# Optimization experiments

Hardware: AMD Instinct MI355X
Metric: run time of the kernel (lower is better)

Reference implementation:

```python
import jax, jax.numpy as jnp
import numpy as np

N_NODES = 50000
X_DIM = 64
EMBED_DIM = 320  # x_dim + hidden*num_hops = 64 + 128*2
N_EDGES = 400000
HIDDEN_MLP = 64
SAMPLE_BIAS = 0.0


def setup_inputs() -> dict:
    key = jax.random.key(0)
    ks = jax.random.split(key, 8)
    x = jax.random.normal(ks[0], (N_NODES, X_DIM), dtype=jnp.float32)
    embed = jax.random.normal(ks[1], (N_NODES, EMBED_DIM), dtype=jnp.float32)
    edge_index = jax.random.randint(ks[2], (2, N_EDGES), 0, N_NODES, dtype=jnp.int64)
    eps = jax.random.uniform(ks[3], (N_EDGES,), dtype=jnp.float32)
    in_channels = 3 * EMBED_DIM
    W1 = jax.random.normal(ks[4], (in_channels, HIDDEN_MLP), dtype=jnp.float32) / np.sqrt(in_channels)
    b1 = jnp.zeros((HIDDEN_MLP,), dtype=jnp.float32)
    W2 = jax.random.normal(ks[5], (HIDDEN_MLP, 1), dtype=jnp.float32) / np.sqrt(HIDDEN_MLP)
    b2 = jnp.zeros((1,), dtype=jnp.float32)
    return {
        'x': x, 'embed': embed, 'edge_index': edge_index, 'node_id': 12345,
        'tmp': jnp.ones((), dtype=jnp.float32), 'eps': eps,
        'W1': W1, 'b1': b1, 'W2': W2, 'b2': b2,
    }


def reference(x, embed, edge_index, node_id, tmp, eps, W1, b1, W2, b2):
    # col, row = edge_index (note: source unpacks col first)
    col = edge_index[0]
    row = edge_index[1]
    E = col.shape[0]
    # gather + concat: [E, 3*embed_dim]
    center = jnp.broadcast_to(embed[node_id][None, :], (E, embed.shape[1]))
    h = jnp.concatenate([embed[col], embed[row], center], axis=-1)
    # 2-layer MLP -> per-edge logit w
    h = jax.nn.relu(h @ W1 + b1)
    w = (h @ W2 + b2).reshape(-1)
    # concrete (Gumbel-sigmoid) relaxation, training=True path
    bias = SAMPLE_BIAS + 0.0001
    e = eps * (1.0 - 2.0 * bias) + bias
    gate = (jnp.log(e) - jnp.log1p(-e) + w) / tmp
    return jax.nn.sigmoid(gate)
```

## Files before the change

kernel.cpp:

```cpp
#include <hip/hip_runtime.h>
#include <math.h>

#define N_NODES   50000
#define EMBED_DIM 320
#define N_EDGES   400000
#define HID       64

typedef __bf16 bf16x8 __attribute__((ext_vector_type(8)));
typedef float  f32x4  __attribute__((ext_vector_type(4)));

__global__ __launch_bounds__(256) void prep_b(const float* __restrict__ W1,
                                              __bf16* __restrict__ Bg) {
    int chunk = blockIdx.x * 256 + threadIdx.x;
    if (chunk >= 5120) return;
    int l  = chunk & 63;
    int sf = chunk >> 6;
    int f  = sf & 7, s = sf >> 3;
    int c  = f * 16 + (l & 15);
    int k0 = s * 32 + (l >> 4) * 8;
    const float* src = W1 + ((size_t)k0 + (c >= 64 ? EMBED_DIM : 0)) * HID + (c & 63);
    __bf16* dst = Bg + (size_t)chunk * 8;
    #pragma unroll
    for (int j = 0; j < 8; ++j) dst[j] = (__bf16)src[(size_t)j * HID];
}

__global__ __launch_bounds__(256) void node_gemm(const float* __restrict__ E,
                                                 const __bf16* __restrict__ Bg,
                                                 const float* __restrict__ W1,
                                                 const float* __restrict__ b1,
                                                 const int* __restrict__ node_id,
                                                 float* __restrict__ P) {
    __shared__ float red[4][64];
    __shared__ float cterm_s[64];
    const int tid = threadIdx.x;

    {
        const int j = tid & 63;
        const int g = tid >> 6;
        const int nid = node_id[0];
        const float* erow = E + (size_t)nid * EMBED_DIM;
        float s = 0.f;
        #pragma unroll 4
        for (int k = g * 80; k < (g + 1) * 80; ++k)
            s = fmaf(erow[k], W1[(size_t)(2 * EMBED_DIM + k) * HID + j], s);
        red[g][j] = s;
    }
    __syncthreads();
    if (tid < 64)
        cterm_s[tid] = b1[tid] + red[0][tid] + red[1][tid] + red[2][tid] + red[3][tid];
    __syncthreads();

    const int wave = tid >> 6;
    const int lane = tid & 63;
    const int r16  = lane & 15;
    const int kg   = lane >> 4;
    const int m0w  = blockIdx.x * 64 + wave * 16;

    int arow_i = m0w + r16;
    if (arow_i > N_NODES - 1) arow_i = N_NODES - 1;
    const float*  arow  = E + (size_t)arow_i * EMBED_DIM + kg * 8;
    const __bf16* bbase = Bg + (size_t)lane * 8;

    f32x4 acc[8] = {};

    float4 aA[2][2];
    bf16x8 bB[2][8];

    aA[0][0] = *(const float4*)(arow + 0);
    aA[0][1] = *(const float4*)(arow + 4);
    #pragma unroll
    for (int f = 0; f < 8; ++f)
        bB[0][f] = *(const bf16x8*)(bbase + (size_t)f * 512);

    #pragma unroll
    for (int s = 0; s < 10; ++s) {
        const int cur = s & 1, nxt = cur ^ 1;
        if (s < 9) {
            const float* an = arow + (s + 1) * 32;
            aA[nxt][0] = *(const float4*)(an + 0);
            aA[nxt][1] = *(const float4*)(an + 4);
            #pragma unroll
            for (int f = 0; f < 8; ++f)
                bB[nxt][f] = *(const bf16x8*)(bbase + (size_t)((s + 1) * 8 + f) * 512);
        }
        bf16x8 av;
        av[0] = (__bf16)aA[cur][0].x; av[1] = (__bf16)aA[cur][0].y;
        av[2] = (__bf16)aA[cur][0].z; av[3] = (__bf16)aA[cur][0].w;
        av[4] = (__bf16)aA[cur][1].x; av[5] = (__bf16)aA[cur][1].y;
        av[6] = (__bf16)aA[cur][1].z; av[7] = (__bf16)aA[cur][1].w;
        #pragma unroll
        for (int f = 0; f < 8; ++f)
            acc[f] = __builtin_amdgcn_mfma_f32_16x16x32_bf16(av, bB[cur][f], acc[f], 0, 0, 0);
    }

    #pragma unroll
    for (int f = 0; f < 8; ++f) {
        float ct = (f < 4) ? cterm_s[f * 16 + r16] : 0.f;
        #pragma unroll
        for (int j = 0; j < 4; ++j) {
            int gr = m0w + kg * 4 + j;
            if (gr < N_NODES)
                P[(size_t)gr * 128 + f * 16 + r16] = acc[f][j] + ct;
        }
    }
}

__global__ __launch_bounds__(256) void edge_kernel(const int* __restrict__ eidx,
                                                   const float* __restrict__ eps,
                                                   const float* __restrict__ P,
                                                   const float* __restrict__ W2,
                                                   const float* __restrict__ b2,
                                                   const float* __restrict__ tmp,
                                                   float* __restrict__ out) {
    const int gid = blockIdx.x * blockDim.x + threadIdx.x;
    const int e   = gid >> 3;
    const int q   = gid & 7;
    if (e >= N_EDGES) return;

    int col = eidx[e];
    int row = eidx[N_EDGES + e];
    col = min(max(col, 0), N_NODES - 1);
    row = min(max(row, 0), N_NODES - 1);

    const float* pc = P + (size_t)col * 128 + q * 8;
    const float* pr = P + (size_t)row * 128 + 64 + q * 8;
    float4 a0 = *(const float4*)(pc + 0);
    float4 a1 = *(const float4*)(pc + 4);
    float4 c0 = *(const float4*)(pr + 0);
    float4 c1 = *(const float4*)(pr + 4);
    float4 w0 = *(const float4*)(W2 + q * 8);
    float4 w1 = *(const float4*)(W2 + q * 8 + 4);

    float s = 0.f;
    s = fmaf(fmaxf(a0.x + c0.x, 0.f), w0.x, s);
    s = fmaf(fmaxf(a0.y + c0.y, 0.f), w0.y, s);
    s = fmaf(fmaxf(a0.z + c0.z, 0.f), w0.z, s);
    s = fmaf(fmaxf(a0.w + c0.w, 0.f), w0.w, s);
    s = fmaf(fmaxf(a1.x + c1.x, 0.f), w1.x, s);
    s = fmaf(fmaxf(a1.y + c1.y, 0.f), w1.y, s);
    s = fmaf(fmaxf(a1.z + c1.z, 0.f), w1.z, s);
    s = fmaf(fmaxf(a1.w + c1.w, 0.f), w1.w, s);

    s += __shfl_xor(s, 1);
    s += __shfl_xor(s, 2);
    s += __shfl_xor(s, 4);

    if (q == 0) {
        float w  = s + b2[0];
        const float bias = 0.0001f;
        float ee = eps[e] * (1.0f - 2.0f * bias) + bias;
        float gate = (logf(ee) - log1pf(-ee) + w) / tmp[0];
        out[e] = 1.0f / (1.0f + expf(-gate));
    }
}

extern "C" void kernel_launch(void* const* d_in, const int* in_sizes, int n_in,
                              void* d_out, int out_size, void* d_ws, size_t ws_size,
                              hipStream_t stream) {
    const float* embed = (const float*)d_in[1];
    const int*   eidx  = (const int*)d_in[2];
    const int*   nid   = (const int*)d_in[3];
    const float* tmp   = (const float*)d_in[4];
    const float* eps   = (const float*)d_in[5];
    const float* W1    = (const float*)d_in[6];
    const float* b1    = (const float*)d_in[7];
    const float* W2    = (const float*)d_in[8];
    const float* b2    = (const float*)d_in[9];
    float*       out   = (float*)d_out;

    float*  P  = (float*)d_ws;
    __bf16* Bg = (__bf16*)((char*)d_ws + (size_t)N_NODES * 128 * sizeof(float));

    prep_b<<<20, 256, 0, stream>>>(W1, Bg);

    int gemm_blocks = (N_NODES + 63) / 64;
    node_gemm<<<gemm_blocks, 256, 0, stream>>>(embed, Bg, W1, b1, nid, P);

    int edge_threads = N_EDGES * 8;
    edge_kernel<<<(edge_threads + 255) / 256, 256, 0, stream>>>(
        eidx, eps, P, W2, b2, tmp, out);
}
```

Before: 173.5 us.

## Store node projections in bf16 and prefetch all A-row loads upfront

The per-node projection table P now holds bf16 instead of fp32. This halves the bytes the GEMM writes and the random gathers the edge kernel reads. Separately, the GEMM now issues all ten A-row fp32 loads at the start rather than double-buffering them, which raises memory-level parallelism at the cost of more registers. The bf16 storage adds rounding error to the pre-activation sums.

```diff
diff --git a/kernel.cpp b/kernel.cpp
--- a/kernel.cpp
+++ b/kernel.cpp
@@ -29,7 +29,7 @@
                                                  const float* __restrict__ W1,
                                                  const float* __restrict__ b1,
                                                  const int* __restrict__ node_id,
-                                                 float* __restrict__ P) {
+                                                 __bf16* __restrict__ P) {
     __shared__ float red[4][64];
     __shared__ float cterm_s[64];
     const int tid = threadIdx.x;
@@ -63,11 +63,14 @@
 
     f32x4 acc[8] = {};
 
-    float4 aA[2][2];
+    float4 aA[10][2];
+    #pragma unroll
+    for (int s = 0; s < 10; ++s) {
+        aA[s][0] = *(const float4*)(arow + s * 32 + 0);
+        aA[s][1] = *(const float4*)(arow + s * 32 + 4);
+    }
+
     bf16x8 bB[2][8];
-
-    aA[0][0] = *(const float4*)(arow + 0);
-    aA[0][1] = *(const float4*)(arow + 4);
     #pragma unroll
     for (int f = 0; f < 8; ++f)
         bB[0][f] = *(const bf16x8*)(bbase + (size_t)f * 512);
@@ -76,18 +79,15 @@
     for (int s = 0; s < 10; ++s) {
         const int cur = s & 1, nxt = cur ^ 1;
         if (s < 9) {
-            const float* an = arow + (s + 1) * 32;
-            aA[nxt][0] = *(const float4*)(an + 0);
-            aA[nxt][1] = *(const float4*)(an + 4);
             #pragma unroll
             for (int f = 0; f < 8; ++f)
                 bB[nxt][f] = *(const bf16x8*)(bbase + (size_t)((s + 1) * 8 + f) * 512);
         }
         bf16x8 av;
-        av[0] = (__bf16)aA[cur][0].x; av[1] = (__bf16)aA[cur][0].y;
-        av[2] = (__bf16)aA[cur][0].z; av[3] = (__bf16)aA[cur][0].w;
-        av[4] = (__bf16)aA[cur][1].x; av[5] = (__bf16)aA[cur][1].y;
-        av[6] = (__bf16)aA[cur][1].z; av[7] = (__bf16)aA[cur][1].w;
+        av[0] = (__bf16)aA[s][0].x; av[1] = (__bf16)aA[s][0].y;
+        av[2] = (__bf16)aA[s][0].z; av[3] = (__bf16)aA[s][0].w;
+        av[4] = (__bf16)aA[s][1].x; av[5] = (__bf16)aA[s][1].y;
+        av[6] = (__bf16)aA[s][1].z; av[7] = (__bf16)aA[s][1].w;
         #pragma unroll
         for (int f = 0; f < 8; ++f)
             acc[f] = __builtin_amdgcn_mfma_f32_16x16x32_bf16(av, bB[cur][f], acc[f], 0, 0, 0);
@@ -100,14 +100,14 @@
         for (int j = 0; j < 4; ++j) {
             int gr = m0w + kg * 4 + j;
             if (gr < N_NODES)
-                P[(size_t)gr * 128 + f * 16 + r16] = acc[f][j] + ct;
+                P[(size_t)gr * 128 + f * 16 + r16] = (__bf16)(acc[f][j] + ct);
         }
     }
 }
 
 __global__ __launch_bounds__(256) void edge_kernel(const int* __restrict__ eidx,
                                                    const float* __restrict__ eps,
-                                                   const float* __restrict__ P,
+                                                   const __bf16* __restrict__ P,
                                                    const float* __restrict__ W2,
                                                    const float* __restrict__ b2,
                                                    const float* __restrict__ tmp,
@@ -122,24 +122,20 @@
     col = min(max(col, 0), N_NODES - 1);
     row = min(max(row, 0), N_NODES - 1);
 
-    const float* pc = P + (size_t)col * 128 + q * 8;
-    const float* pr = P + (size_t)row * 128 + 64 + q * 8;
-    float4 a0 = *(const float4*)(pc + 0);
-    float4 a1 = *(const float4*)(pc + 4);
-    float4 c0 = *(const float4*)(pr + 0);
-    float4 c1 = *(const float4*)(pr + 4);
+    bf16x8 a = *(const bf16x8*)(P + (size_t)col * 128 + q * 8);
+    bf16x8 c = *(const bf16x8*)(P + (size_t)row * 128 + 64 + q * 8);
     float4 w0 = *(const float4*)(W2 + q * 8);
     float4 w1 = *(const float4*)(W2 + q * 8 + 4);
 
     float s = 0.f;
-    s = fmaf(fmaxf(a0.x + c0.x, 0.f), w0.x, s);
-    s = fmaf(fmaxf(a0.y + c0.y, 0.f), w0.y, s);
-    s = fmaf(fmaxf(a0.z + c0.z, 0.f), w0.z, s);
-    s = fmaf(fmaxf(a0.w + c0.w, 0.f), w0.w, s);
-    s = fmaf(fmaxf(a1.x + c1.x, 0.f), w1.x, s);
-    s = fmaf(fmaxf(a1.y + c1.y, 0.f), w1.y, s);
-    s = fmaf(fmaxf(a1.z + c1.z, 0.f), w1.z, s);
-    s = fmaf(fmaxf(a1.w + c1.w, 0.f), w1.w, s);
+    s = fmaf(fmaxf((float)a[0] + (float)c[0], 0.f), w0.x, s);
+    s = fmaf(fmaxf((float)a[1] + (float)c[1], 0.f), w0.y, s);
+    s = fmaf(fmaxf((float)a[2] + (float)c[2], 0.f), w0.z, s);
+    s = fmaf(fmaxf((float)a[3] + (float)c[3], 0.f), w0.w, s);
+    s = fmaf(fmaxf((float)a[4] + (float)c[4], 0.f), w1.x, s);
+    s = fmaf(fmaxf((float)a[5] + (float)c[5], 0.f), w1.y, s);
+    s = fmaf(fmaxf((float)a[6] + (float)c[6], 0.f), w1.z, s);
+    s = fmaf(fmaxf((float)a[7] + (float)c[7], 0.f), w1.w, s);
 
     s += __shfl_xor(s, 1);
     s += __shfl_xor(s, 2);
@@ -168,8 +164,8 @@
     const float* b2    = (const float*)d_in[9];
     float*       out   = (float*)d_out;
 
-    float*  P  = (float*)d_ws;
-    __bf16* Bg = (__bf16*)((char*)d_ws + (size_t)N_NODES * 128 * sizeof(float));
+    __bf16* P  = (__bf16*)d_ws;
+    __bf16* Bg = (__bf16*)((char*)d_ws + (size_t)N_NODES * 128 * sizeof(__bf16));
 
     prep_b<<<20, 256, 0, stream>>>(W1, Bg);
 
```

Measured after the change: 162.6 us. 6.3% less time.
